# Kernel optimization log

Hardware: AMD Instinct MI355X
Metric: run time of the kernel (lower is better)

## Reference

```python
import jax, jax.numpy as jnp
import numpy as np

B, S, D_MODEL = 2, 2048, 2048
N_HEADS, N_KV = 32, 8
HEAD_DIM = D_MODEL // N_HEADS          # 64
HPG = N_HEADS // N_KV                  # heads per group = 4
DIM_K = HEAD_DIM * N_KV                # 512 (used as softmax scale per original code)


def setup_inputs() -> dict:
    key = jax.random.key(0)
    ks = jax.random.split(key, 11)
    s = lambda fan_in: 1.0 / np.sqrt(fan_in)
    return {
        "inputs_q": jax.random.normal(ks[0], (B, S, D_MODEL), jnp.float32),
        "inputs_k": jax.random.normal(ks[1], (B, S, D_MODEL), jnp.float32),
        "inputs_v": jax.random.normal(ks[2], (B, S, D_MODEL), jnp.float32),
        "Wq": jax.random.normal(ks[3], (D_MODEL, D_MODEL), jnp.float32) * s(D_MODEL),
        "bq": jnp.zeros((D_MODEL,), jnp.float32),
        "Wk": jax.random.normal(ks[4], (D_MODEL, DIM_K), jnp.float32) * s(D_MODEL),
        "bk": jnp.zeros((DIM_K,), jnp.float32),
        "Wv": jax.random.normal(ks[5], (D_MODEL, DIM_K), jnp.float32) * s(D_MODEL),
        "bv": jnp.zeros((DIM_K,), jnp.float32),
        "Wo": jax.random.normal(ks[6], (D_MODEL, D_MODEL), jnp.float32) * s(D_MODEL),
        "bo": jnp.zeros((D_MODEL,), jnp.float32),
    }


def reference(inputs_q, inputs_k, inputs_v, Wq, bq, Wk, bk, Wv, bv, Wo, bo):
    b, s, _ = inputs_q.shape
    q = inputs_q @ Wq + bq                       # [B,S,dim_q]
    k = inputs_k @ Wk + bk                       # [B,S,dim_k]
    v = inputs_v @ Wv + bv                       # [B,S,dim_v]
    q = q.reshape(b, s, N_KV, HPG, HEAD_DIM)     # b m g p d
    k = k.reshape(b, s, N_KV, HEAD_DIM)          # b n g d
    v = v.reshape(b, s, N_KV, HEAD_DIM)          # b n g d
    # logits[b,g,p,m,n] = q . k ; scale by sqrt(dim_k) per original code
    logits = jnp.einsum('bmgpd,bngd->bgpmn', q, k) / jnp.sqrt(jnp.float32(DIM_K))
    # causal mask (lower triangular allowed)
    causal = jnp.tril(jnp.ones((s, s), bool))
    logits = jnp.where(causal, logits, -jnp.inf)
    attn = jax.nn.softmax(logits, axis=-1)       # [B,G,P,M,N]
    out = jnp.einsum('bgpmn,bngd->bmgpd', attn, v)
    out = out.reshape(b, s, N_KV * HPG * HEAD_DIM)
    return out @ Wo + bo
```

## Files before the change

### kernel.cpp

```cpp
#include <hip/hip_runtime.h>
#include <hip/hip_bf16.h>

typedef __hip_bfloat16 bf16;
typedef float f32x4 __attribute__((ext_vector_type(4)));
typedef float f32x16 __attribute__((ext_vector_type(16)));
typedef short bf16x8 __attribute__((ext_vector_type(8)));

#define B_   2
#define S_   2048
#define DM   2048
#define HD   64
#define NH   32

__device__ __forceinline__ void async16(void* lds, const void* g) {
  __builtin_amdgcn_global_load_lds(
      (const __attribute__((address_space(1))) unsigned int*)g,
      (__attribute__((address_space(3))) unsigned int*)lds, 16, 0, 0);
}

template <int N> __device__ __forceinline__ void waitvm() {
  asm volatile("s_waitcnt vmcnt(%0)" :: "i"(N) : "memory");
}

__device__ __forceinline__ float exp2a(float x) {
  float r; asm("v_exp_f32 %0, %1" : "=v"(r) : "v"(x)); return r;
}
__device__ __forceinline__ unsigned cvtpk(float lo, float hi) {
  unsigned r; asm("v_cvt_pk_bf16_f32 %0, %1, %2" : "=v"(r) : "v"(lo), "v"(hi)); return r;
}
__device__ __forceinline__ void perm32swap(unsigned &a, unsigned &b) {
  asm volatile("v_permlane32_swap_b32 %0, %1" : "+v"(a), "+v"(b));
}

__global__ __launch_bounds__(256)
void prep_kernel(const float* __restrict__ xq, const float* __restrict__ xk,
                 const float* __restrict__ xv,
                 const float* __restrict__ Wq, const float* __restrict__ Wo,
                 const float* __restrict__ Wk, const float* __restrict__ Wv,
                 const float* __restrict__ bk, const float* __restrict__ bv,
                 bf16* __restrict__ Xq, bf16* __restrict__ Xk, bf16* __restrict__ Xv,
                 bf16* __restrict__ WqT, bf16* __restrict__ WoT, bf16* __restrict__ WkvT,
                 float* __restrict__ bkv) {
  const int blk = blockIdx.x;
  const int tid = threadIdx.x;

  if (blk < 12288) {
    const int a = blk >> 12;
    const int r = blk & 4095;
    const float* in = (a == 0) ? xq : (a == 1) ? xk : xv;
    bf16* out = (a == 0) ? Xq : (a == 1) ? Xk : Xv;
    const size_t i = ((size_t)r * 256 + tid) * 8;
    float4 v0 = *(const float4*)(in + i);
    float4 v1 = *(const float4*)(in + i + 4);
    union { bf16 h[8]; uint4 v; } u;
    u.h[0] = __float2bfloat16(v0.x); u.h[1] = __float2bfloat16(v0.y);
    u.h[2] = __float2bfloat16(v0.z); u.h[3] = __float2bfloat16(v0.w);
    u.h[4] = __float2bfloat16(v1.x); u.h[5] = __float2bfloat16(v1.y);
    u.h[6] = __float2bfloat16(v1.z); u.h[7] = __float2bfloat16(v1.w);
    *(uint4*)(out + i) = u.v;
    return;
  }

  int t = blk - 12288;
  const float* W; bf16* Wt; int N;
  if (t < 4096)       { W = Wq; Wt = WqT; N = 2048; }
  else if (t < 8192)  { t -= 4096; W = Wo; Wt = WoT; N = 2048; }
  else if (t < 9216)  { t -= 8192; W = Wk; Wt = WkvT; N = 512; }
  else if (t < 10240) { t -= 9216; W = Wv; Wt = WkvT + (size_t)512 * 2048; N = 512; }
  else {
    #pragma unroll
    for (int j = 0; j < 4; ++j) {
      const int i = tid * 4 + j;
      bkv[i] = (i < 512) ? bk[i] : bv[i - 512];
    }
    return;
  }
  const int k0 = (t & 63) * 32, n0 = (t >> 6) * 32;
  __shared__ float tile[32][33];
  const int tx = tid & 31, ty = tid >> 5;
  #pragma unroll
  for (int i = 0; i < 32; i += 8)
    tile[ty + i][tx] = W[(size_t)(k0 + ty + i) * N + n0 + tx];
  __syncthreads();
  #pragma unroll
  for (int i = 0; i < 32; i += 8)
    Wt[(size_t)(n0 + ty + i) * 2048 + k0 + tx] = __float2bfloat16(tile[tx][ty + i]);
}

__device__ __forceinline__ void store_out(float* C, size_t idx, float v) { C[idx] = v; }
__device__ __forceinline__ void store_out(bf16* C, size_t idx, float v) { C[idx] = __float2bfloat16(v); }

template <typename OUT>
__device__ __forceinline__ void gemm_body(const bf16* __restrict__ Au,
                                          const bf16* __restrict__ Bt,
                                          const float* __restrict__ bias, float omul,
                                          OUT* __restrict__ C, int N, int m0, int n0,
                                          bf16* As, bf16* Bs) {
  constexpr int BK = 32;
  const int tid = threadIdx.x;
  const int wave = tid >> 6, lane = tid & 63;
  const int l15 = lane & 15, l4 = lane >> 4;
  const int wm = (wave & 1) * 64, wn = (wave >> 1) * 64;

  f32x4 acc[4][4] = {};
  const int nk = 2048 / BK;

  auto stage = [&](int kt, int buf) {
    const int k0 = kt * BK;
    #pragma unroll
    for (int i = 0; i < 2; ++i) {
      const int rb = wave * 32 + i * 16;
      const int r  = rb + (lane >> 2);
      const int cs = (lane & 3) ^ ((r >> 1) & 3);
      async16(As + buf * 4096 + rb * BK, Au + (size_t)(m0 + r) * 2048 + k0 + cs * 8);
      async16(Bs + buf * 4096 + rb * BK, Bt + (size_t)(n0 + r) * 2048 + k0 + cs * 8);
    }
  };

  stage(0, 0);
  asm volatile("s_waitcnt vmcnt(0)" ::: "memory");
  __syncthreads();

  for (int kt = 0; kt < nk; ++kt) {
    const int cur = kt & 1;
    if (kt + 1 < nk) stage(kt + 1, cur ^ 1);
    bf16x8 af[4], bfr[4];
    #pragma unroll
    for (int f = 0; f < 4; ++f) {
      const int mr = wm + f * 16 + l15;
      af[f]  = *(const bf16x8*)(As + cur * 4096 + mr * BK + (l4 ^ ((mr >> 1) & 3)) * 8);
      const int nr = wn + f * 16 + l15;
      bfr[f] = *(const bf16x8*)(Bs + cur * 4096 + nr * BK + (l4 ^ ((nr >> 1) & 3)) * 8);
    }
    __builtin_amdgcn_s_setprio(1);
    #pragma unroll
    for (int i = 0; i < 4; ++i)
      #pragma unroll
      for (int j = 0; j < 4; ++j)
        acc[i][j] = __builtin_amdgcn_mfma_f32_16x16x32_bf16(af[i], bfr[j], acc[i][j], 0, 0, 0);
    __builtin_amdgcn_s_setprio(0);
    asm volatile("s_waitcnt vmcnt(0)" ::: "memory");
    __syncthreads();
  }

  const int r0 = m0 + wm + l4 * 4;
  const int c0 = n0 + wn + l15;
  #pragma unroll
  for (int j = 0; j < 4; ++j) {
    const int col = c0 + j * 16;
    const float bb = bias[col];
    #pragma unroll
    for (int i = 0; i < 4; ++i)
      #pragma unroll
      for (int r = 0; r < 4; ++r)
        store_out(C, (size_t)(r0 + i * 16 + r) * N + col, (acc[i][j][r] + bb) * omul);
  }
}

__global__ __launch_bounds__(256)
void gemm_qkv(const bf16* __restrict__ Xq, const bf16* __restrict__ Xk,
              const bf16* __restrict__ Xv,
              const bf16* __restrict__ WqT, const bf16* __restrict__ WkvT,
              const float* __restrict__ bq, const float* __restrict__ bkv,
              bf16* __restrict__ Qb, bf16* __restrict__ KVb) {
  __shared__ __align__(16) bf16 As[2][128 * 32];
  __shared__ __align__(16) bf16 Bs[2][128 * 32];
  const int bid = blockIdx.x;
  const int wg = (bid & 7) * 96 + (bid >> 3);
  if (wg < 512) {
    gemm_body<bf16>(Xq, WqT, bq, 0.063758717f, Qb, 2048,
                    (wg & 31) * 128, (wg >> 5) * 128, &As[0][0], &Bs[0][0]);
  } else {
    const int b2 = wg - 512;
    const int m0 = (b2 & 31) * 128, n0 = (b2 >> 5) * 128;
    gemm_body<bf16>(n0 < 512 ? Xk : Xv, WkvT, bkv, 1.0f, KVb, 1024,
                    m0, n0, &As[0][0], &Bs[0][0]);
  }
}

__global__ __launch_bounds__(256)
void gemm_o(const bf16* __restrict__ AO, const bf16* __restrict__ WoT,
            const float* __restrict__ bo, float* __restrict__ out) {
  __shared__ __align__(16) bf16 As[2][128 * 32];
  __shared__ __align__(16) bf16 Bs[2][128 * 32];
  gemm_body<float>(AO, WoT, bo, 1.0f, out, 2048,
                   blockIdx.x * 128, blockIdx.y * 128, &As[0][0], &Bs[0][0]);
}

__global__ __launch_bounds__(256, 3)
void attn_kernel(const bf16* __restrict__ Q, const bf16* __restrict__ KV, bf16* __restrict__ O) {
  const int pair = blockIdx.x, h = blockIdx.y, b = blockIdx.z;
  const int g = h >> 2;
  const int tid = threadIdx.x;
  const int wave = tid >> 6, lane = tid & 63;
  const int l31 = lane & 31, l5 = lane >> 5;

  __shared__ __align__(16) char smem[40960];
  bf16* KsBuf = (bf16*)smem;
  bf16* VtBuf = (bf16*)(smem + 24576);
  char* ob = smem + wave * 4608;

  const bf16* KVb = KV + (size_t)(b * S_) * 1024;
  const int kcol = g * HD;
  const int vcol = 512 + g * HD;
  const int kv2 = tid & 31, vd0 = (tid >> 5) * 8;

  auto stageK = [&](int buf, int kv0) {
    #pragma unroll
    for (int i2 = 0; i2 < 2; ++i2) {
      const int rb = wave * 16 + i2 * 8;
      const int r = rb + (lane >> 3);
      const int cs = (lane & 7) ^ (r & 7);
      async16(KsBuf + buf * 4096 + rb * 64, KVb + (size_t)(kv0 + r) * 1024 + kcol + cs * 8);
    }
  };
  auto writeV = [&](int buf, uint4 va, uint4 vb) {
    const unsigned short* a0 = (const unsigned short*)&va;
    const unsigned short* a1 = (const unsigned short*)&vb;
    char* base = (char*)VtBuf + buf * 8192;
    #pragma unroll
    for (int j = 0; j < 8; ++j) {
      unsigned val = (unsigned)a0[j] | ((unsigned)a1[j] << 16);
      const int d = vd0 + j;
      *(unsigned*)(base + d * 128 + ((kv2 * 4) ^ ((d & 7) << 4))) = val;
    }
  };

  for (int sub = 0; sub < 2; ++sub) {
    const int qt = (sub == 0) ? pair : 15 - pair;
    const int qbase = qt * 128;
    const int nt = 2 * qt + 2;
    const int qrow = qbase + wave * 32 + l31;
    const int wmax = qbase + wave * 32 + 31;

    bf16x8 qf[4];
    const bf16* qp = Q + (size_t)(b * S_ + qrow) * DM + h * HD + l5 * 8;
    #pragma unroll
    for (int ks = 0; ks < 4; ++ks) qf[ks] = *(const bf16x8*)(qp + ks * 16);

    f32x16 ot[2] = {};
    float m = -3.0e38f, lsum = 0.f;
    uint4 vr0, vr1;

    {
      const bf16* vp = KVb + (size_t)(2 * kv2) * 1024 + vcol + vd0;
      vr0 = *(const uint4*)vp;
      vr1 = *(const uint4*)(vp + 1024);
    }
    stageK(0, 0);
    stageK(1, 64);
    waitvm<4>();
    writeV(0, vr0, vr1);
    waitvm<2>();
    asm volatile("s_waitcnt lgkmcnt(0)" ::: "memory");
    __builtin_amdgcn_s_barrier();
    asm volatile("" ::: "memory");

    for (int t = 0; t < nt; ++t) {
      const int kv0 = t * 64;
      if (t + 1 < nt) {
        const bf16* vp = KVb + (size_t)((t + 1) * 64 + 2 * kv2) * 1024 + vcol + vd0;
        vr0 = *(const uint4*)vp;
        vr1 = *(const uint4*)(vp + 1024);
      }
      if (t + 2 < nt) stageK((t + 2) % 3, (t + 2) * 64);

      if (kv0 <= wmax) {
        const char* kb = (const char*)(KsBuf + (t % 3) * 4096);
        const char* vb = (const char*)(VtBuf + (t & 1) * 4096);
        f32x16 sT[2] = {};
        __builtin_amdgcn_s_setprio(1);
        #pragma unroll
        for (int ks = 0; ks < 4; ++ks) {
          #pragma unroll
          for (int i = 0; i < 2; ++i) {
            const int row = i * 32 + l31;
            bf16x8 kf = *(const bf16x8*)(kb + row * 128 +
                                         ((ks * 32 + l5 * 16) ^ ((row & 7) << 4)));
            sT[i] = __builtin_amdgcn_mfma_f32_32x32x16_bf16(kf, qf[ks], sT[i], 0, 0, 0);
          }
        }
        __builtin_amdgcn_s_setprio(0);
        if (kv0 + 63 > qbase + wave * 32) {
          #pragma unroll
          for (int i = 0; i < 2; ++i)
            #pragma unroll
            for (int r = 0; r < 16; ++r) {
              const int kvg = kv0 + i * 32 + ((r & 3) + 8 * (r >> 2)) + 4 * l5;
              if (kvg > qrow) sT[i][r] = -3.0e38f;
            }
        }
        float a16[16];
        #pragma unroll
        for (int r = 0; r < 16; ++r) a16[r] = fmaxf(sT[0][r], sT[1][r]);
        #pragma unroll
        for (int s2 = 8; s2 >= 1; s2 >>= 1)
          #pragma unroll
          for (int r = 0; r < 8; ++r) if (r < s2) a16[r] = fmaxf(a16[r], a16[r + s2]);
        float pm = fmaxf(a16[0], __shfl_xor(a16[0], 32));
        if (!__all(pm - m <= 8.f)) {
          const float mn = fmaxf(m, pm);
          const float alpha = exp2a(m - mn);
          m = mn;
          lsum *= alpha;
          #pragma unroll
          for (int r = 0; r < 16; ++r) { ot[0][r] *= alpha; ot[1][r] *= alpha; }
        }
        float rs0 = 0.f, rs1 = 0.f;
        unsigned pk[2][8];
        #pragma unroll
        for (int i = 0; i < 2; ++i)
          #pragma unroll
          for (int rr = 0; rr < 8; ++rr) {
            const float p0 = exp2a(sT[i][2 * rr] - m);
            const float p1 = exp2a(sT[i][2 * rr + 1] - m);
            if (i == 0) rs0 += p0 + p1; else rs1 += p0 + p1;
            pk[i][rr] = cvtpk(p0, p1);
          }
        float rs = rs0 + rs1;
        rs += __shfl_xor(rs, 32);
        lsum += rs;
        #pragma unroll
        for (int i = 0; i < 2; ++i) {
          #pragma unroll
          for (int kp = 0; kp < 2; ++kp) {
            unsigned w0 = pk[i][4 * kp + 0], w1 = pk[i][4 * kp + 1];
            unsigned w2 = pk[i][4 * kp + 2], w3 = pk[i][4 * kp + 3];
            perm32swap(w0, w2);
            perm32swap(w1, w3);
            union { unsigned u[4]; bf16x8 v; } pf = {{w0, w1, w2, w3}};
            const int ks2 = i * 2 + kp;
            __builtin_amdgcn_s_setprio(1);
            #pragma unroll
            for (int f = 0; f < 2; ++f) {
              const int row = f * 32 + l31;
              bf16x8 vf = *(const bf16x8*)(vb + row * 128 +
                                           ((ks2 * 32 + l5 * 16) ^ ((row & 7) << 4)));
              ot[f] = __builtin_amdgcn_mfma_f32_32x32x16_bf16(vf, pf.v, ot[f], 0, 0, 0);
            }
            __builtin_amdgcn_s_setprio(0);
          }
        }
      }

      if (t + 2 < nt) waitvm<2>();
      else            waitvm<0>();
      if (t + 1 < nt) writeV((t + 1) & 1, vr0, vr1);
      asm volatile("s_waitcnt lgkmcnt(0)" ::: "memory");
      __builtin_amdgcn_s_barrier();
      asm volatile("" ::: "memory");
    }

    const float inv = 1.0f / lsum;
    #pragma unroll
    for (int f = 0; f < 2; ++f)
      #pragma unroll
      for (int g2 = 0; g2 < 4; ++g2) {
        uint2 val;
        val.x = cvtpk(ot[f][g2 * 4 + 0] * inv, ot[f][g2 * 4 + 1] * inv);
        val.y = cvtpk(ot[f][g2 * 4 + 2] * inv, ot[f][g2 * 4 + 3] * inv);
        *(uint2*)(ob + l31 * 144 + f * 64 + g2 * 16 + l5 * 8) = val;
      }
    asm volatile("s_waitcnt lgkmcnt(0)" ::: "memory");
    __builtin_amdgcn_sched_barrier(0);
    #pragma unroll
    for (int rr = 0; rr < 4; ++rr) {
      const int row = rr * 8 + (lane >> 3);
      uint4 dv = *(const uint4*)(ob + row * 144 + (lane & 7) * 16);
      *(uint4*)(O + (size_t)(b * S_ + qbase + wave * 32 + row) * DM + h * HD + (lane & 7) * 8) = dv;
    }
    __syncthreads();
  }
}

extern "C" void kernel_launch(void* const* d_in, const int* in_sizes, int n_in,
                              void* d_out, int out_size, void* d_ws, size_t ws_size,
                              hipStream_t stream) {
  const float* xq = (const float*)d_in[0];
  const float* xk = (const float*)d_in[1];
  const float* xv = (const float*)d_in[2];
  const float* Wq = (const float*)d_in[3];
  const float* bq = (const float*)d_in[4];
  const float* Wk = (const float*)d_in[5];
  const float* bk = (const float*)d_in[6];
  const float* Wv = (const float*)d_in[7];
  const float* bv = (const float*)d_in[8];
  const float* Wo = (const float*)d_in[9];
  const float* bo = (const float*)d_in[10];
  float* out = (float*)d_out;

  char* ws = (char*)d_ws;
  bf16*  Xq   = (bf16*)(ws);
  bf16*  Xk   = (bf16*)(ws + 16777216);
  bf16*  Xv   = (bf16*)(ws + 33554432);
  bf16*  WqT  = (bf16*)(ws + 50331648);
  bf16*  WkvT = (bf16*)(ws + 58720256);
  bf16*  WoT  = (bf16*)(ws + 62914560);
  float* bkv  = (float*)(ws + 71303168);
  bf16*  Qb   = (bf16*)(ws + 71307264);
  bf16*  KVb  = (bf16*)(ws + 88084480);
  bf16*  AO   = Xq;

  prep_kernel<<<22529, 256, 0, stream>>>(xq, xk, xv, Wq, Wo, Wk, Wv, bk, bv,
                                         Xq, Xk, Xv, WqT, WoT, WkvT, bkv);
  gemm_qkv<<<768, 256, 0, stream>>>(Xq, Xk, Xv, WqT, WkvT, bq, bkv, Qb, KVb);
  attn_kernel<<<dim3(8, 32, 2), 256, 0, stream>>>(Qb, KVb, AO);
  gemm_o<<<dim3(32, 16), 256, 0, stream>>>(AO, WoT, bo, out);
}
```

Baseline: 231.9 us.

## Stage 128-row KV tiles per barrier in attention kernel

The attention loop now stages K and V in 128-row tiles instead of 64, processing two 64-row sub-steps per tile. This halves the number of block barriers and wait points per query tile. The transposed V layout is widened with a new swizzle, and each thread loads 32 bytes per V row pair. Shared memory doubles to 80 KB, which may cut occupancy below the launch-bounds target of 3 blocks.

```diff
diff --git a/kernel.cpp b/kernel.cpp
--- a/kernel.cpp
+++ b/kernel.cpp
@@ -195,41 +195,48 @@
   const int wave = tid >> 6, lane = tid & 63;
   const int l31 = lane & 31, l5 = lane >> 5;
 
-  __shared__ __align__(16) char smem[40960];
-  bf16* KsBuf = (bf16*)smem;
-  bf16* VtBuf = (bf16*)(smem + 24576);
-  char* ob = smem + wave * 4608;
+  __shared__ __align__(16) char smem[81920];
+  char* KsB = smem;
+  char* VtB = smem + 49152;
+  char* ob  = smem + wave * 4608;
 
   const bf16* KVb = KV + (size_t)(b * S_) * 1024;
   const int kcol = g * HD;
   const int vcol = 512 + g * HD;
-  const int kv2 = tid & 31, vd0 = (tid >> 5) * 8;
+  const int kvp = lane;
+  const int vd0 = wave * 16;
 
   auto stageK = [&](int buf, int kv0) {
     #pragma unroll
-    for (int i2 = 0; i2 < 2; ++i2) {
-      const int rb = wave * 16 + i2 * 8;
+    for (int i2 = 0; i2 < 4; ++i2) {
+      const int rb = wave * 32 + i2 * 8;
       const int r = rb + (lane >> 3);
       const int cs = (lane & 7) ^ (r & 7);
-      async16(KsBuf + buf * 4096 + rb * 64, KVb + (size_t)(kv0 + r) * 1024 + kcol + cs * 8);
+      async16(KsB + buf * 16384 + rb * 128, KVb + (size_t)(kv0 + r) * 1024 + kcol + cs * 8);
     }
   };
-  auto writeV = [&](int buf, uint4 va, uint4 vb) {
-    const unsigned short* a0 = (const unsigned short*)&va;
-    const unsigned short* a1 = (const unsigned short*)&vb;
-    char* base = (char*)VtBuf + buf * 8192;
-    #pragma unroll
-    for (int j = 0; j < 8; ++j) {
-      unsigned val = (unsigned)a0[j] | ((unsigned)a1[j] << 16);
-      const int d = vd0 + j;
-      *(unsigned*)(base + d * 128 + ((kv2 * 4) ^ ((d & 7) << 4))) = val;
+  auto loadV = [&](int kv0, uint4* vr) {
+    const bf16* vp = KVb + (size_t)(kv0 + 2 * kvp) * 1024 + vcol + vd0;
+    vr[0] = *(const uint4*)vp;
+    vr[1] = *(const uint4*)(vp + 8);
+    vr[2] = *(const uint4*)(vp + 1024);
+    vr[3] = *(const uint4*)(vp + 1032);
+  };
+  auto writeV = [&](int buf, const uint4* vr) {
+    const unsigned short* r0 = (const unsigned short*)&vr[0];
+    const unsigned short* r1 = (const unsigned short*)&vr[2];
+    char* base = VtB + buf * 16384;
+    #pragma unroll
+    for (int j = 0; j < 16; ++j) {
+      unsigned val = (unsigned)r0[j] | ((unsigned)r1[j] << 16);
+      *(unsigned*)(base + (vd0 + j) * 256 + ((kvp * 4) ^ (j << 4))) = val;
     }
   };
 
   for (int sub = 0; sub < 2; ++sub) {
     const int qt = (sub == 0) ? pair : 15 - pair;
     const int qbase = qt * 128;
-    const int nt = 2 * qt + 2;
+    const int n = qt + 1;
     const int qrow = qbase + wave * 32 + l31;
     const int wmax = qbase + wave * 32 + 31;
 
@@ -240,54 +247,49 @@
 
     f32x16 ot[2] = {};
     float m = -3.0e38f, lsum = 0.f;
-    uint4 vr0, vr1;
-
-    {
-      const bf16* vp = KVb + (size_t)(2 * kv2) * 1024 + vcol + vd0;
-      vr0 = *(const uint4*)vp;
-      vr1 = *(const uint4*)(vp + 1024);
-    }
+    uint4 vr[4];
+
+    loadV(0, vr);
     stageK(0, 0);
-    stageK(1, 64);
-    waitvm<4>();
-    writeV(0, vr0, vr1);
-    waitvm<2>();
+    if (n > 1) stageK(1, 128);
+    if (n > 1) waitvm<8>(); else waitvm<4>();
+    writeV(0, vr);
+    if (n > 1) waitvm<4>(); else waitvm<0>();
     asm volatile("s_waitcnt lgkmcnt(0)" ::: "memory");
     __builtin_amdgcn_s_barrier();
     asm volatile("" ::: "memory");
 
-    for (int t = 0; t < nt; ++t) {
-      const int kv0 = t * 64;
-      if (t + 1 < nt) {
-        const bf16* vp = KVb + (size_t)((t + 1) * 64 + 2 * kv2) * 1024 + vcol + vd0;
-        vr0 = *(const uint4*)vp;
-        vr1 = *(const uint4*)(vp + 1024);
-      }
-      if (t + 2 < nt) stageK((t + 2) % 3, (t + 2) * 64);
-
-      if (kv0 <= wmax) {
-        const char* kb = (const char*)(KsBuf + (t % 3) * 4096);
-        const char* vb = (const char*)(VtBuf + (t & 1) * 4096);
+    for (int i = 0; i < n; ++i) {
+      if (i + 1 < n) loadV((i + 1) * 128, vr);
+      if (i + 2 < n) stageK((i + 2) % 3, (i + 2) * 128);
+
+      const char* kbuf = KsB + (i % 3) * 16384;
+      const char* vbuf = VtB + (i & 1) * 16384;
+
+      #pragma unroll
+      for (int hh = 0; hh < 2; ++hh) {
+        const int kv0 = i * 128 + hh * 64;
+        if (kv0 > wmax) break;
         f32x16 sT[2] = {};
         __builtin_amdgcn_s_setprio(1);
         #pragma unroll
         for (int ks = 0; ks < 4; ++ks) {
           #pragma unroll
-          for (int i = 0; i < 2; ++i) {
-            const int row = i * 32 + l31;
-            bf16x8 kf = *(const bf16x8*)(kb + row * 128 +
-                                         ((ks * 32 + l5 * 16) ^ ((row & 7) << 4)));
-            sT[i] = __builtin_amdgcn_mfma_f32_32x32x16_bf16(kf, qf[ks], sT[i], 0, 0, 0);
+          for (int f = 0; f < 2; ++f) {
+            const int rL = hh * 64 + f * 32 + l31;
+            bf16x8 kf = *(const bf16x8*)(kbuf + rL * 128 +
+                                         ((ks * 32 + l5 * 16) ^ ((rL & 7) << 4)));
+            sT[f] = __builtin_amdgcn_mfma_f32_32x32x16_bf16(kf, qf[ks], sT[f], 0, 0, 0);
           }
         }
         __builtin_amdgcn_s_setprio(0);
         if (kv0 + 63 > qbase + wave * 32) {
           #pragma unroll
-          for (int i = 0; i < 2; ++i)
+          for (int f = 0; f < 2; ++f)
             #pragma unroll
             for (int r = 0; r < 16; ++r) {
-              const int kvg = kv0 + i * 32 + ((r & 3) + 8 * (r >> 2)) + 4 * l5;
-              if (kvg > qrow) sT[i][r] = -3.0e38f;
+              const int kvg = kv0 + f * 32 + ((r & 3) + 8 * (r >> 2)) + 4 * l5;
+              if (kvg > qrow) sT[f][r] = -3.0e38f;
             }
         }
         float a16[16];
@@ -309,33 +311,33 @@
         float rs0 = 0.f, rs1 = 0.f;
         unsigned pk[2][8];
         #pragma unroll
-        for (int i = 0; i < 2; ++i)
+        for (int f = 0; f < 2; ++f)
           #pragma unroll
           for (int rr = 0; rr < 8; ++rr) {
-            const float p0 = exp2a(sT[i][2 * rr] - m);
-            const float p1 = exp2a(sT[i][2 * rr + 1] - m);
-            if (i == 0) rs0 += p0 + p1; else rs1 += p0 + p1;
-            pk[i][rr] = cvtpk(p0, p1);
+            const float p0 = exp2a(sT[f][2 * rr] - m);
+            const float p1 = exp2a(sT[f][2 * rr + 1] - m);
+            if (f == 0) rs0 += p0 + p1; else rs1 += p0 + p1;
+            pk[f][rr] = cvtpk(p0, p1);
           }
         float rs = rs0 + rs1;
         rs += __shfl_xor(rs, 32);
         lsum += rs;
         #pragma unroll
-        for (int i = 0; i < 2; ++i) {
+        for (int f2 = 0; f2 < 2; ++f2) {
           #pragma unroll
           for (int kp = 0; kp < 2; ++kp) {
-            unsigned w0 = pk[i][4 * kp + 0], w1 = pk[i][4 * kp + 1];
-            unsigned w2 = pk[i][4 * kp + 2], w3 = pk[i][4 * kp + 3];
+            unsigned w0 = pk[f2][4 * kp + 0], w1 = pk[f2][4 * kp + 1];
+            unsigned w2 = pk[f2][4 * kp + 2], w3 = pk[f2][4 * kp + 3];
             perm32swap(w0, w2);
             perm32swap(w1, w3);
             union { unsigned u[4]; bf16x8 v; } pf = {{w0, w1, w2, w3}};
-            const int ks2 = i * 2 + kp;
+            const int ks2 = f2 * 2 + kp;
             __builtin_amdgcn_s_setprio(1);
             #pragma unroll
             for (int f = 0; f < 2; ++f) {
-              const int row = f * 32 + l31;
-              bf16x8 vf = *(const bf16x8*)(vb + row * 128 +
-                                           ((ks2 * 32 + l5 * 16) ^ ((row & 7) << 4)));
+              const int d = f * 32 + l31;
+              bf16x8 vf = *(const bf16x8*)(vbuf + d * 256 +
+                             ((hh * 128 + ks2 * 32 + l5 * 16) ^ ((d & 15) << 4)));
               ot[f] = __builtin_amdgcn_mfma_f32_32x32x16_bf16(vf, pf.v, ot[f], 0, 0, 0);
             }
             __builtin_amdgcn_s_setprio(0);
@@ -343,9 +345,11 @@
         }
       }
 
-      if (t + 2 < nt) waitvm<2>();
-      else            waitvm<0>();
-      if (t + 1 < nt) writeV((t + 1) & 1, vr0, vr1);
+      if (i + 1 < n) {
+        if (i + 2 < n) waitvm<4>();
+        else           waitvm<0>();
+        writeV((i + 1) & 1, vr);
+      }
       asm volatile("s_waitcnt lgkmcnt(0)" ::: "memory");
       __builtin_amdgcn_s_barrier();
       asm volatile("" ::: "memory");
```

Result: slower. 276.5 us (+19.3%).
